# Kernel optimization log

Hardware: AMD Instinct MI355X
Metric: run time of the kernel (lower is better)

## Reference

```python
import jax, jax.numpy as jnp
import numpy as np

N, M, D_IN, D_TXT, D_OUT, H = 4096, 1024, 512, 512, 512, 8
DH = D_OUT // H


def positional_encoding(n, dim):
    # Matches PositionalEncoding: freq = exp((arange(dim//2)/dim)*ln(10000)),
    # x = pos/freq -> [L, dim//2], interleave (sin, cos) pairs -> [L, dim].
    pos = jnp.arange(n, dtype=jnp.float32)
    freq = jnp.exp((jnp.arange(dim // 2, dtype=jnp.float32) / dim) * jnp.log(jnp.float32(10000.0)))
    x = pos[:, None] / freq  # [L, dim//2]
    pe = jnp.stack((jnp.sin(x), jnp.cos(x)), axis=-1)  # [L, dim//2, 2]
    return pe.reshape(n, dim)


def setup_inputs() -> dict:
    key = jax.random.key(0)
    k1, k2, k3, k4, k5, k6 = jax.random.split(key, 6)
    s = 0.02
    return {
        "video_features": jax.random.normal(k1, (N, D_IN), dtype=jnp.float32),
        "text_features": jax.random.normal(k2, (M, D_TXT), dtype=jnp.float32),
        "Wq": jax.random.normal(k3, (H, D_IN, DH), dtype=jnp.float32) * s,
        "Wk": jax.random.normal(k4, (H, D_TXT, DH), dtype=jnp.float32) * s,
        "Wv": jax.random.normal(k5, (H, D_TXT, DH), dtype=jnp.float32) * s,
        "Wout": jax.random.normal(k6, (D_OUT, D_IN), dtype=jnp.float32) * s,
    }


def reference(video_features, text_features, Wq, Wk, Wv, Wout):
    # Batched over heads instead of the original per-head Python loop (same math).
    Q = jnp.einsum('nd,hde->hne', video_features, Wq)   # [H, N, DH]
    K = jnp.einsum('md,hde->hme', text_features, Wk)    # [H, M, DH]
    V = jnp.einsum('md,hde->hme', text_features, Wv)    # [H, M, DH]
    energies = jnp.einsum('hne,hme->hnm', Q, K)         # no scaling in original
    att = jax.nn.softmax(energies, axis=-1)             # dropout omitted (eval mode)
    y = jnp.einsum('hnm,hme->hne', att, V)              # [H, N, DH]
    y = jnp.transpose(y, (1, 0, 2)).reshape(video_features.shape[0], -1)  # concat heads
    y = y @ Wout                                        # [N, D_IN]
    y = y + positional_encoding(y.shape[0], y.shape[1])
    return y
```

## Files before the change

kernel.cpp:

```cpp
#include <hip/hip_runtime.h>
#include <hip/hip_bf16.h>
#include <math.h>

#define N_TOK 4096
#define M_TOK 1024
#define DMODEL 512
#define NHEAD 8
#define DHEAD 64

typedef __attribute__((ext_vector_type(8))) short short8;
typedef __attribute__((ext_vector_type(4))) float f32x4;
typedef __attribute__((ext_vector_type(4))) float float4v;

static __device__ __forceinline__ short f2bf(float f) {
    union { float f; unsigned u; } v; v.f = f;
    unsigned r = v.u + 0x7fffu + ((v.u >> 16) & 1u);
    return (short)(r >> 16);
}

#define GLOAD_LDS16(g, l) __builtin_amdgcn_global_load_lds( \
    (const __attribute__((address_space(1))) void*)(g), \
    (__attribute__((address_space(3))) void*)(l), 16, 0, 0)

__global__ void pack_kernel(const float* __restrict__ xv, const float* __restrict__ xt,
                            const float* __restrict__ wq, const float* __restrict__ wk,
                            const float* __restrict__ wv, const float* __restrict__ wo,
                            short* __restrict__ xvb, short* __restrict__ xtb,
                            short* __restrict__ wqb, short* __restrict__ wkb,
                            short* __restrict__ wvb, short* __restrict__ wob) {
    int idx = blockIdx.x * 256 + threadIdx.x;
    int stride = gridDim.x * 256;
    const int CXV = N_TOK * DMODEL / 8;
    const int CXT = M_TOK * DMODEL / 8;
    const int NW  = DMODEL * DMODEL;
    for (int c = idx; c < CXV; c += stride) {
        float4v f0 = *(const float4v*)&xv[c * 8];
        float4v f1 = *(const float4v*)&xv[c * 8 + 4];
        short8 o;
        #pragma unroll
        for (int j = 0; j < 4; j++) { o[j] = f2bf(f0[j]); o[j + 4] = f2bf(f1[j]); }
        *(short8*)&xvb[c * 8] = o;
    }
    for (int c = idx; c < CXT; c += stride) {
        float4v f0 = *(const float4v*)&xt[c * 8];
        float4v f1 = *(const float4v*)&xt[c * 8 + 4];
        short8 o;
        #pragma unroll
        for (int j = 0; j < 4; j++) { o[j] = f2bf(f0[j]); o[j + 4] = f2bf(f1[j]); }
        *(short8*)&xtb[c * 8] = o;
    }
    for (int i = idx; i < NW; i += stride) {
        int n = i >> 9;
        int k = i & 511;
        int h = n >> 6, e = n & 63;
        int src = h * (DMODEL * DHEAD) + k * DHEAD + e;
        wqb[i] = f2bf(wq[src]);
        wkb[i] = f2bf(wk[src]);
        wvb[i] = f2bf(wv[src]);
        wob[i] = f2bf(wo[k * DMODEL + n]);
    }
}

__global__ __launch_bounds__(256) void gemmQKV(const short* __restrict__ xvb,
                                               const short* __restrict__ xtb,
                                               const short* __restrict__ wqb,
                                               const short* __restrict__ wkb,
                                               const short* __restrict__ wvb,
                                               short* __restrict__ qb,
                                               short* __restrict__ kbm,
                                               short* __restrict__ vbt) {
    __shared__ __align__(16) short As[64][72];
    __shared__ __align__(16) short Bs[64][72];
    int bx = blockIdx.x;
    const short* A; const short* BT; short* C; int m0; bool transC;
    if (bx < 64)      { A = xvb; BT = wqb; C = qb;  m0 = bx * 64;        transC = false; }
    else if (bx < 80) { A = xtb; BT = wkb; C = kbm; m0 = (bx - 64) * 64; transC = false; }
    else              { A = xtb; BT = wvb; C = vbt; m0 = (bx - 80) * 64; transC = true;  }
    int n0 = blockIdx.y * 64;
    int t = threadIdx.x;
    int lane = t & 63, w = t >> 6;
    int wr = w >> 1, wc = w & 1;
    int l15 = lane & 15, g = lane >> 4;

    f32x4 acc[2][2] = {};
    for (int kk = 0; kk < DMODEL; kk += 64) {
        {
            int row = t >> 2, c0 = (t & 3) * 16;
            *(short8*)&As[row][c0]     = *(const short8*)&A[(m0 + row) * DMODEL + kk + c0];
            *(short8*)&As[row][c0 + 8] = *(const short8*)&A[(m0 + row) * DMODEL + kk + c0 + 8];
            *(short8*)&Bs[row][c0]     = *(const short8*)&BT[(n0 + row) * DMODEL + kk + c0];
            *(short8*)&Bs[row][c0 + 8] = *(const short8*)&BT[(n0 + row) * DMODEL + kk + c0 + 8];
        }
        __syncthreads();
        #pragma unroll
        for (int ks = 0; ks < 2; ks++) {
            short8 a[2], b[2];
            #pragma unroll
            for (int fr = 0; fr < 2; fr++) a[fr] = *(short8*)&As[wr * 32 + fr * 16 + l15][ks * 32 + g * 8];
            #pragma unroll
            for (int fc = 0; fc < 2; fc++) b[fc] = *(short8*)&Bs[wc * 32 + fc * 16 + l15][ks * 32 + g * 8];
            #pragma unroll
            for (int fr = 0; fr < 2; fr++)
                #pragma unroll
                for (int fc = 0; fc < 2; fc++)
                    acc[fr][fc] = __builtin_amdgcn_mfma_f32_16x16x32_bf16(a[fr], b[fc], acc[fr][fc], 0, 0, 0);
        }
        __syncthreads();
    }
    #pragma unroll
    for (int fr = 0; fr < 2; fr++)
        #pragma unroll
        for (int fc = 0; fc < 2; fc++)
            #pragma unroll
            for (int r = 0; r < 4; r++) {
                int row = m0 + wr * 32 + fr * 16 + g * 4 + r;
                int col = n0 + wc * 32 + fc * 16 + l15;
                float v = acc[fr][fc][r];
                if (transC) C[col * M_TOK + row] = f2bf(v);
                else        C[row * DMODEL + col] = f2bf(v);
            }
}

__global__ __launch_bounds__(256) void gemmOut(const short* __restrict__ A,
                                               const short* __restrict__ BT,
                                               float* __restrict__ Cout) {
    __shared__ __align__(16) short As[64][72];
    __shared__ __align__(16) short Bs[64][72];
    __shared__ float ifreq[256];
    int m0 = blockIdx.x * 64;
    int n0 = blockIdx.y * 64;
    int t = threadIdx.x;
    int lane = t & 63, w = t >> 6;
    int wr = w >> 1, wc = w & 1;
    int l15 = lane & 15, g = lane >> 4;

    ifreq[t] = expf(-(float)t * (9.210340371976184f / 512.0f));

    f32x4 acc[2][2] = {};
    for (int kk = 0; kk < DMODEL; kk += 64) {
        {
            int row = t >> 2, c0 = (t & 3) * 16;
            *(short8*)&As[row][c0]     = *(const short8*)&A[(m0 + row) * DMODEL + kk + c0];
            *(short8*)&As[row][c0 + 8] = *(const short8*)&A[(m0 + row) * DMODEL + kk + c0 + 8];
            *(short8*)&Bs[row][c0]     = *(const short8*)&BT[(n0 + row) * DMODEL + kk + c0];
            *(short8*)&Bs[row][c0 + 8] = *(const short8*)&BT[(n0 + row) * DMODEL + kk + c0 + 8];
        }
        __syncthreads();
        #pragma unroll
        for (int ks = 0; ks < 2; ks++) {
            short8 a[2], b[2];
            #pragma unroll
            for (int fr = 0; fr < 2; fr++) a[fr] = *(short8*)&As[wr * 32 + fr * 16 + l15][ks * 32 + g * 8];
            #pragma unroll
            for (int fc = 0; fc < 2; fc++) b[fc] = *(short8*)&Bs[wc * 32 + fc * 16 + l15][ks * 32 + g * 8];
            #pragma unroll
            for (int fr = 0; fr < 2; fr++)
                #pragma unroll
                for (int fc = 0; fc < 2; fc++)
                    acc[fr][fc] = __builtin_amdgcn_mfma_f32_16x16x32_bf16(a[fr], b[fc], acc[fr][fc], 0, 0, 0);
        }
        __syncthreads();
    }
    #pragma unroll
    for (int fr = 0; fr < 2; fr++)
        #pragma unroll
        for (int fc = 0; fc < 2; fc++)
            #pragma unroll
            for (int r = 0; r < 4; r++) {
                int row = m0 + wr * 32 + fr * 16 + g * 4 + r;
                int col = n0 + wc * 32 + fc * 16 + l15;
                float x = (float)row * ifreq[col >> 1];
                float pe = (col & 1) ? cosf(x) : sinf(x);
                Cout[row * DMODEL + col] = acc[fr][fc][r] + pe;
            }
}

__global__ __launch_bounds__(256) void attn_kernel(const short* __restrict__ Qb,
                                                   const short* __restrict__ Kb,
                                                   const short* __restrict__ VbT,
                                                   short* __restrict__ Yb) {
    __shared__ __align__(16) short Ks[2][64][64];
    __shared__ __align__(16) short Vs[2][64][64];
    __shared__ __align__(16) short Ps[4][16][72];

    int bid = blockIdx.x;
    int h = bid & 7;
    int qx = bid >> 3;
    int n0 = qx * 64;
    int t = threadIdx.x;
    int lane = t & 63, w = t >> 6;
    int l15 = lane & 15, g = lane >> 4;

    const short* Kh  = Kb + h * DHEAD;
    const short* VhT = VbT + (h * DHEAD) * M_TOK;

    int srow = (lane >> 3);
    int sgran = (lane & 7) ^ srow;
    const short* gK0 = Kh + (size_t)(w * 16 + srow) * DMODEL + sgran * 8;
    const short* gV0 = VhT + (size_t)(w * 16 + srow) * M_TOK + sgran * 8;

    const short* qrow = Qb + (size_t)(n0 + w * 16 + l15) * DMODEL + h * DHEAD;
    short8 qa0 = *(const short8*)(qrow + g * 8);
    short8 qa1 = *(const short8*)(qrow + 32 + g * 8);

    f32x4 acc[4] = {};
    f32x4 rsum = {};
    int sx = l15 & 7;

    {
        GLOAD_LDS16(gK0,                 &Ks[0][w * 16][0]);
        GLOAD_LDS16(gK0 + 8 * DMODEL,    &Ks[0][w * 16 + 8][0]);
        GLOAD_LDS16(gV0,                 &Vs[0][w * 16][0]);
        GLOAD_LDS16(gV0 + 8 * M_TOK,     &Vs[0][w * 16 + 8][0]);
    }
    __syncthreads();

    int buf = 0;
    for (int it = 0; it < 16; ++it) {
        if (it < 15) {
            int key0 = (it + 1) * 64;
            GLOAD_LDS16(gK0 + (size_t)key0 * DMODEL,             &Ks[buf ^ 1][w * 16][0]);
            GLOAD_LDS16(gK0 + (size_t)(key0 + 8) * DMODEL,       &Ks[buf ^ 1][w * 16 + 8][0]);
            GLOAD_LDS16(gV0 + key0,                              &Vs[buf ^ 1][w * 16][0]);
            GLOAD_LDS16(gV0 + key0 + 8 * M_TOK,                  &Vs[buf ^ 1][w * 16 + 8][0]);
        }
        #pragma unroll
        for (int kt = 0; kt < 4; kt++) {
            short8 kf0 = *(short8*)&Ks[buf][kt * 16 + l15][((g) ^ sx) * 8];
            short8 kf1 = *(short8*)&Ks[buf][kt * 16 + l15][((4 + g) ^ sx) * 8];
            f32x4 e = {};
            e = __builtin_amdgcn_mfma_f32_16x16x32_bf16(qa0, kf0, e, 0, 0, 0);
            e = __builtin_amdgcn_mfma_f32_16x16x32_bf16(qa1, kf1, e, 0, 0, 0);
            #pragma unroll
            for (int r = 0; r < 4; r++) {
                float p = exp2f(e[r] * 1.44269504f);
                rsum[r] += p;
                Ps[w][g * 4 + r][kt * 16 + l15] = f2bf(p);
            }
        }
        #pragma unroll
        for (int kb2 = 0; kb2 < 2; kb2++) {
            short8 pa = *(short8*)&Ps[w][l15][kb2 * 32 + g * 8];
            #pragma unroll
            for (int nt = 0; nt < 4; nt++) {
                short8 vf = *(short8*)&Vs[buf][nt * 16 + l15][((kb2 * 4 + g) ^ sx) * 8];
                acc[nt] = __builtin_amdgcn_mfma_f32_16x16x32_bf16(pa, vf, acc[nt], 0, 0, 0);
            }
        }
        __syncthreads();
        buf ^= 1;
    }

    #pragma unroll
    for (int r = 0; r < 4; r++) {
        float s = rsum[r];
        s += __shfl_xor(s, 1);
        s += __shfl_xor(s, 2);
        s += __shfl_xor(s, 4);
        s += __shfl_xor(s, 8);
        rsum[r] = s;
    }

    #pragma unroll
    for (int nt = 0; nt < 4; nt++)
        #pragma unroll
        for (int r = 0; r < 4; r++) {
            float y = acc[nt][r] / rsum[r];
            Yb[(size_t)(n0 + w * 16 + g * 4 + r) * DMODEL + h * DHEAD + nt * 16 + l15] = f2bf(y);
        }
}

extern "C" void kernel_launch(void* const* d_in, const int* in_sizes, int n_in,
                              void* d_out, int out_size, void* d_ws, size_t ws_size,
                              hipStream_t stream) {
    const float* xv = (const float*)d_in[0];
    const float* xt = (const float*)d_in[1];
    const float* wq = (const float*)d_in[2];
    const float* wk = (const float*)d_in[3];
    const float* wv = (const float*)d_in[4];
    const float* wo = (const float*)d_in[5];

    short* xvb = (short*)d_ws;
    short* xtb = xvb + N_TOK * DMODEL;
    short* wqb = xtb + M_TOK * DMODEL;
    short* wkb = wqb + DMODEL * DMODEL;
    short* wvb = wkb + DMODEL * DMODEL;
    short* wob = wvb + DMODEL * DMODEL;
    short* qb  = wob + DMODEL * DMODEL;
    short* kbm = qb  + N_TOK * DMODEL;
    short* vbt = kbm + M_TOK * DMODEL;
    short* yb  = vbt + M_TOK * DMODEL;

    pack_kernel<<<1024, 256, 0, stream>>>(xv, xt, wq, wk, wv, wo,
                                          xvb, xtb, wqb, wkb, wvb, wob);
    gemmQKV<<<dim3(96, 8), 256, 0, stream>>>(xvb, xtb, wqb, wkb, wvb, qb, kbm, vbt);
    attn_kernel<<<512, 256, 0, stream>>>(qb, kbm, vbt, yb);
    gemmOut<<<dim3(N_TOK / 64, 8), 256, 0, stream>>>(yb, wob, (float*)d_out);
}
```

Baseline: 61.86 us.

## Share a double-buffered async-LDS GEMM body with swizzled tiles across projections

Replaces both GEMM kernels with a shared templated body that uses 128x64 tiles, direct global-to-LDS loads, double buffering and an XOR-swizzled LDS layout without padding. The goal is to overlap global loads with MFMA work, remove the register round-trip when staging tiles, and avoid LDS bank conflicts. Each warp now computes a 32x64 strip, which halves the number of blocks (384 for QKV, 256 for the output GEMM). The trade-off is lower block-level parallelism and more LDS per block.

```diff
diff --git a/kernel.cpp b/kernel.cpp
--- a/kernel.cpp
+++ b/kernel.cpp
@@ -61,6 +61,70 @@
     }
 }
 
+template<typename EPI>
+static __device__ __forceinline__ void gemm_body(const short* __restrict__ A,
+                                                 const short* __restrict__ BT,
+                                                 int m0, int n0, EPI epi) {
+    __shared__ __align__(16) short As[2][128][64];
+    __shared__ __align__(16) short Bs[2][64][64];
+    int t = threadIdx.x;
+    int lane = t & 63, w = t >> 6;
+    int l15 = lane & 15, g = lane >> 4;
+    int srow = lane >> 3;
+    int sgran = (lane & 7) ^ (srow & 7);
+    int sx = l15 & 7;
+
+    const short* gA = A + (size_t)(m0 + w * 32 + srow) * DMODEL + sgran * 8;
+    const short* gB = BT + (size_t)(n0 + w * 16 + srow) * DMODEL + sgran * 8;
+
+    f32x4 acc[2][4] = {};
+
+    #pragma unroll
+    for (int i = 0; i < 4; i++) GLOAD_LDS16(gA + (size_t)(i * 8) * DMODEL, &As[0][w * 32 + i * 8][0]);
+    #pragma unroll
+    for (int i = 0; i < 2; i++) GLOAD_LDS16(gB + (size_t)(i * 8) * DMODEL, &Bs[0][w * 16 + i * 8][0]);
+    __syncthreads();
+
+    int buf = 0;
+    for (int ks_step = 0; ks_step < DMODEL / 64; ++ks_step) {
+        if (ks_step < DMODEL / 64 - 1) {
+            int kk = (ks_step + 1) * 64;
+            #pragma unroll
+            for (int i = 0; i < 4; i++) GLOAD_LDS16(gA + (size_t)(i * 8) * DMODEL + kk, &As[buf ^ 1][w * 32 + i * 8][0]);
+            #pragma unroll
+            for (int i = 0; i < 2; i++) GLOAD_LDS16(gB + (size_t)(i * 8) * DMODEL + kk, &Bs[buf ^ 1][w * 16 + i * 8][0]);
+        }
+        #pragma unroll
+        for (int ks = 0; ks < 2; ks++) {
+            short8 a[2], b[4];
+            #pragma unroll
+            for (int fr = 0; fr < 2; fr++)
+                a[fr] = *(short8*)&As[buf][w * 32 + fr * 16 + l15][((ks * 4 + g) ^ sx) * 8];
+            #pragma unroll
+            for (int fc = 0; fc < 4; fc++)
+                b[fc] = *(short8*)&Bs[buf][fc * 16 + l15][((ks * 4 + g) ^ sx) * 8];
+            #pragma unroll
+            for (int fr = 0; fr < 2; fr++)
+                #pragma unroll
+                for (int fc = 0; fc < 4; fc++)
+                    acc[fr][fc] = __builtin_amdgcn_mfma_f32_16x16x32_bf16(a[fr], b[fc], acc[fr][fc], 0, 0, 0);
+        }
+        __syncthreads();
+        buf ^= 1;
+    }
+
+    #pragma unroll
+    for (int fr = 0; fr < 2; fr++)
+        #pragma unroll
+        for (int fc = 0; fc < 4; fc++)
+            #pragma unroll
+            for (int r = 0; r < 4; r++) {
+                int row = m0 + w * 32 + fr * 16 + g * 4 + r;
+                int col = n0 + fc * 16 + l15;
+                epi(row, col, acc[fr][fc][r]);
+            }
+}
+
 __global__ __launch_bounds__(256) void gemmQKV(const short* __restrict__ xvb,
                                                const short* __restrict__ xtb,
                                                const short* __restrict__ wqb,
@@ -69,110 +133,37 @@
                                                short* __restrict__ qb,
                                                short* __restrict__ kbm,
                                                short* __restrict__ vbt) {
-    __shared__ __align__(16) short As[64][72];
-    __shared__ __align__(16) short Bs[64][72];
     int bx = blockIdx.x;
-    const short* A; const short* BT; short* C; int m0; bool transC;
-    if (bx < 64)      { A = xvb; BT = wqb; C = qb;  m0 = bx * 64;        transC = false; }
-    else if (bx < 80) { A = xtb; BT = wkb; C = kbm; m0 = (bx - 64) * 64; transC = false; }
-    else              { A = xtb; BT = wvb; C = vbt; m0 = (bx - 80) * 64; transC = true;  }
-    int n0 = blockIdx.y * 64;
-    int t = threadIdx.x;
-    int lane = t & 63, w = t >> 6;
-    int wr = w >> 1, wc = w & 1;
-    int l15 = lane & 15, g = lane >> 4;
-
-    f32x4 acc[2][2] = {};
-    for (int kk = 0; kk < DMODEL; kk += 64) {
-        {
-            int row = t >> 2, c0 = (t & 3) * 16;
-            *(short8*)&As[row][c0]     = *(const short8*)&A[(m0 + row) * DMODEL + kk + c0];
-            *(short8*)&As[row][c0 + 8] = *(const short8*)&A[(m0 + row) * DMODEL + kk + c0 + 8];
-            *(short8*)&Bs[row][c0]     = *(const short8*)&BT[(n0 + row) * DMODEL + kk + c0];
-            *(short8*)&Bs[row][c0 + 8] = *(const short8*)&BT[(n0 + row) * DMODEL + kk + c0 + 8];
-        }
-        __syncthreads();
-        #pragma unroll
-        for (int ks = 0; ks < 2; ks++) {
-            short8 a[2], b[2];
-            #pragma unroll
-            for (int fr = 0; fr < 2; fr++) a[fr] = *(short8*)&As[wr * 32 + fr * 16 + l15][ks * 32 + g * 8];
-            #pragma unroll
-            for (int fc = 0; fc < 2; fc++) b[fc] = *(short8*)&Bs[wc * 32 + fc * 16 + l15][ks * 32 + g * 8];
-            #pragma unroll
-            for (int fr = 0; fr < 2; fr++)
-                #pragma unroll
-                for (int fc = 0; fc < 2; fc++)
-                    acc[fr][fc] = __builtin_amdgcn_mfma_f32_16x16x32_bf16(a[fr], b[fc], acc[fr][fc], 0, 0, 0);
-        }
-        __syncthreads();
-    }
-    #pragma unroll
-    for (int fr = 0; fr < 2; fr++)
-        #pragma unroll
-        for (int fc = 0; fc < 2; fc++)
-            #pragma unroll
-            for (int r = 0; r < 4; r++) {
-                int row = m0 + wr * 32 + fr * 16 + g * 4 + r;
-                int col = n0 + wc * 32 + fc * 16 + l15;
-                float v = acc[fr][fc][r];
-                if (transC) C[col * M_TOK + row] = f2bf(v);
-                else        C[row * DMODEL + col] = f2bf(v);
-            }
+    if (bx < 256) {
+        short* C = qb;
+        gemm_body(xvb, wqb, (bx >> 3) * 128, (bx & 7) * 64,
+                  [&](int row, int col, float v) { C[(size_t)row * DMODEL + col] = f2bf(v); });
+    } else if (bx < 320) {
+        int b = bx - 256;
+        short* C = kbm;
+        gemm_body(xtb, wkb, (b >> 3) * 128, (b & 7) * 64,
+                  [&](int row, int col, float v) { C[(size_t)row * DMODEL + col] = f2bf(v); });
+    } else {
+        int b = bx - 320;
+        short* C = vbt;
+        gemm_body(xtb, wvb, (b >> 3) * 128, (b & 7) * 64,
+                  [&](int row, int col, float v) { C[(size_t)col * M_TOK + row] = f2bf(v); });
+    }
 }
 
 __global__ __launch_bounds__(256) void gemmOut(const short* __restrict__ A,
                                                const short* __restrict__ BT,
                                                float* __restrict__ Cout) {
-    __shared__ __align__(16) short As[64][72];
-    __shared__ __align__(16) short Bs[64][72];
     __shared__ float ifreq[256];
-    int m0 = blockIdx.x * 64;
-    int n0 = blockIdx.y * 64;
-    int t = threadIdx.x;
-    int lane = t & 63, w = t >> 6;
-    int wr = w >> 1, wc = w & 1;
-    int l15 = lane & 15, g = lane >> 4;
-
-    ifreq[t] = expf(-(float)t * (9.210340371976184f / 512.0f));
-
-    f32x4 acc[2][2] = {};
-    for (int kk = 0; kk < DMODEL; kk += 64) {
-        {
-            int row = t >> 2, c0 = (t & 3) * 16;
-            *(short8*)&As[row][c0]     = *(const short8*)&A[(m0 + row) * DMODEL + kk + c0];
-            *(short8*)&As[row][c0 + 8] = *(const short8*)&A[(m0 + row) * DMODEL + kk + c0 + 8];
-            *(short8*)&Bs[row][c0]     = *(const short8*)&BT[(n0 + row) * DMODEL + kk + c0];
-            *(short8*)&Bs[row][c0 + 8] = *(const short8*)&BT[(n0 + row) * DMODEL + kk + c0 + 8];
-        }
-        __syncthreads();
-        #pragma unroll
-        for (int ks = 0; ks < 2; ks++) {
-            short8 a[2], b[2];
-            #pragma unroll
-            for (int fr = 0; fr < 2; fr++) a[fr] = *(short8*)&As[wr * 32 + fr * 16 + l15][ks * 32 + g * 8];
-            #pragma unroll
-            for (int fc = 0; fc < 2; fc++) b[fc] = *(short8*)&Bs[wc * 32 + fc * 16 + l15][ks * 32 + g * 8];
-            #pragma unroll
-            for (int fr = 0; fr < 2; fr++)
-                #pragma unroll
-                for (int fc = 0; fc < 2; fc++)
-                    acc[fr][fc] = __builtin_amdgcn_mfma_f32_16x16x32_bf16(a[fr], b[fc], acc[fr][fc], 0, 0, 0);
-        }
-        __syncthreads();
-    }
-    #pragma unroll
-    for (int fr = 0; fr < 2; fr++)
-        #pragma unroll
-        for (int fc = 0; fc < 2; fc++)
-            #pragma unroll
-            for (int r = 0; r < 4; r++) {
-                int row = m0 + wr * 32 + fr * 16 + g * 4 + r;
-                int col = n0 + wc * 32 + fc * 16 + l15;
-                float x = (float)row * ifreq[col >> 1];
-                float pe = (col & 1) ? cosf(x) : sinf(x);
-                Cout[row * DMODEL + col] = acc[fr][fc][r] + pe;
-            }
+    ifreq[threadIdx.x] = expf(-(float)threadIdx.x * (9.210340371976184f / 512.0f));
+    __syncthreads();
+    int bx = blockIdx.x;
+    gemm_body(A, BT, (bx >> 3) * 128, (bx & 7) * 64,
+              [&](int row, int col, float v) {
+                  float x = (float)row * ifreq[col >> 1];
+                  float pe = (col & 1) ? cosf(x) : sinf(x);
+                  Cout[(size_t)row * DMODEL + col] = v + pe;
+              });
 }
 
 __global__ __launch_bounds__(256) void attn_kernel(const short* __restrict__ Qb,
@@ -293,7 +284,7 @@
 
     pack_kernel<<<1024, 256, 0, stream>>>(xv, xt, wq, wk, wv, wo,
                                           xvb, xtb, wqb, wkb, wvb, wob);
-    gemmQKV<<<dim3(96, 8), 256, 0, stream>>>(xvb, xtb, wqb, wkb, wvb, qb, kbm, vbt);
+    gemmQKV<<<384, 256, 0, stream>>>(xvb, xtb, wqb, wkb, wvb, qb, kbm, vbt);
     attn_kernel<<<512, 256, 0, stream>>>(qb, kbm, vbt, yb);
-    gemmOut<<<dim3(N_TOK / 64, 8), 256, 0, stream>>>(yb, wob, (float*)d_out);
-}
+    gemmOut<<<256, 256, 0, stream>>>(yb, wob, (float*)d_out);
+}
```

Measured after the change: 72.31 us. 16.9% more time.
